# Kernel tuning notes

Measured on AMD Instinct MI355X. Metric: run time of the kernel, lower is better.

The kernel has to match this reference:

```python
import jax, jax.numpy as jnp
import numpy as np

# Model config (matches init_kwargs)
L, B, S, D, H, HKV, HD, FF, V = 2, 1, 2048, 2048, 16, 4, 128, 5632, 32000
EPS = 1e-5
ROPE_BASE = 10000.0


def setup_inputs() -> dict:
    key = jax.random.key(0)
    ks = jax.random.split(key, 13)
    s = 0.02  # init scale keeps activations/softmax numerically sane
    return {
        "idx": jax.random.randint(ks[0], (B, S), 0, V, dtype=jnp.int32),
        "embed": jax.random.normal(ks[1], (V, D), jnp.float32) * s,
        "wq": jax.random.normal(ks[2], (L, D, D), jnp.float32) * s,
        "wk": jax.random.normal(ks[3], (L, D, HKV * HD), jnp.float32) * s,
        "wv": jax.random.normal(ks[4], (L, D, HKV * HD), jnp.float32) * s,
        "wo": jax.random.normal(ks[5], (L, D, D), jnp.float32) * s,
        "ln1_g": jnp.ones((L, D), jnp.float32),
        "ln2_g": jnp.ones((L, D), jnp.float32),
        "w_gate": jax.random.normal(ks[6], (L, D, FF), jnp.float32) * s,
        "w_up": jax.random.normal(ks[7], (L, D, FF), jnp.float32) * s,
        "w_down": jax.random.normal(ks[8], (L, FF, D), jnp.float32) * s,
        "final_g": jnp.ones((D,), jnp.float32),
        "lm_head": jax.random.normal(ks[9], (V, D), jnp.float32) * s,
    }


def _rope_cos_sin(seq_len, n_elem, base=ROPE_BASE):
    inv = 1.0 / base ** (jnp.arange(0, n_elem, 2, dtype=jnp.float32)[: n_elem // 2] / n_elem)
    f = jnp.outer(jnp.arange(seq_len, dtype=jnp.float32), inv)  # [S, HD/2]
    return jnp.cos(f), jnp.sin(f)


def _apply_rope(x, cos, sin):
    # x: [B, S, h, HD]; split last dim into halves (matches torch reshape(...,2,-1))
    d2 = x.shape[-1] // 2
    x1, x2 = x[..., :d2], x[..., d2:]
    c = cos[None, :, None, :]
    s = sin[None, :, None, :]
    return jnp.concatenate([x1 * c - x2 * s, x2 * c + x1 * s], axis=-1)


def _rmsnorm(x, g, eps=EPS):
    return x * jax.lax.rsqrt(jnp.mean(x * x, axis=-1, keepdims=True) + eps) * g


def _forward(idx, embed, wq, wk, wv, wo, ln1_g, ln2_g, w_gate, w_up, w_down, final_g, lm_head):
    cos, sin = _rope_cos_sin(S, HD)
    # NOTE: the original uses a MULTIPLICATIVE bool mask on scores (scores * mask),
    # zeroing (not -inf'ing) future positions before softmax. Replicated faithfully.
    mask = jnp.tril(jnp.ones((S, S), jnp.float32))
    rep = H // HKV
    scale = 1.0 / np.sqrt(HD).astype(np.float32)

    x = embed[idx]  # [B, S, D]

    def layer(x, p):
        lwq, lwk, lwv, lwo, g1, g2, lwg, lwu, lwd = p
        h = _rmsnorm(x, g1)
        q = (h @ lwq).reshape(B, S, H, HD)
        k = (h @ lwk).reshape(B, S, HKV, HD)
        v = (h @ lwv).reshape(B, S, HKV, HD)
        q = _apply_rope(q, cos, sin)
        k = _apply_rope(k, cos, sin)
        k = jnp.repeat(k, rep, axis=2)  # GQA repeat_interleave over heads
        v = jnp.repeat(v, rep, axis=2)
        scores = jnp.einsum("bqhd,bkhd->bhqk", q, k) * scale * mask
        attn = jax.nn.softmax(scores, axis=-1)
        y = jnp.einsum("bhqk,bkhd->bqhd", attn, v).reshape(B, S, D) @ lwo
        x = x + y
        h2 = _rmsnorm(x, g2)
        x = x + (jax.nn.silu(h2 @ lwu) * (h2 @ lwg)) @ lwd
        return x, None

    x, _ = jax.lax.scan(layer, x, (wq, wk, wv, wo, ln1_g, ln2_g, w_gate, w_up, w_down))
    return _rmsnorm(x, final_g) @ lm_head.T  # [B, S, V]


def reference(idx, embed, wq, wk, wv, wo, ln1_g, ln2_g, w_gate, w_up, w_down, final_g, lm_head):
    return _forward(idx, embed, wq, wk, wv, wo, ln1_g, ln2_g, w_gate, w_up, w_down, final_g, lm_head)
```

## Files before the change

### kernel.cpp

```cpp
#include <hip/hip_runtime.h>

#define SQ     2048
#define DMODEL 2048
#define NHEAD  16
#define NKV    4
#define HDIM   128
#define FFDIM  5632
#define VOCAB  32000
#define NLAYER 2
#define EPSV   1e-5f

typedef __bf16 bf16;
typedef __bf16 bf16x4 __attribute__((ext_vector_type(4)));
typedef __bf16 bf16x8 __attribute__((ext_vector_type(8)));
typedef float  f32x4  __attribute__((ext_vector_type(4)));

enum { EP_STOREF = 0, EP_ADD = 2, EP_STOREB = 3, EP_QKV = 6, EP_GLU = 7, EP_ATOMIC = 8 };

#define GLD(gp, lp) __builtin_amdgcn_global_load_lds( \
    (const __attribute__((address_space(1))) void*)(gp), \
    (__attribute__((address_space(3))) void*)(lp), 16, 0, 0)

#define MFMA16(a, b, c) __builtin_amdgcn_mfma_f32_16x16x32_bf16(a, b, c, 0, 0, 0)

#define FENCE() __builtin_amdgcn_sched_barrier(0)
#define PH_BAR() do { FENCE(); __builtin_amdgcn_s_barrier(); FENCE(); } while (0)

#define XCD_SWZ(TM)                                                        \
  const int GM  = (int)gridDim.x;                                          \
  const int nwg = GM * (int)gridDim.y;                                     \
  const int bid = (int)blockIdx.y * GM + (int)blockIdx.x;                  \
  const int q8  = nwg >> 3, r8 = nwg & 7;                                  \
  const int xcd = bid & 7, rnk = bid >> 3;                                 \
  const int swz = ((xcd < r8) ? xcd * (q8 + 1)                             \
                              : r8 * (q8 + 1) + (xcd - r8) * q8) + rnk;    \
  const int m0  = (swz % GM) * (TM);                                       \
  const int n0  = (swz / GM) * (TM == 256 ? 256 : 128);

template<int EPI, int NBUF>
__global__ __launch_bounds__(256, NBUF == 2 ? 2 : 1)
void gemm128(const bf16* __restrict__ A, const bf16* __restrict__ B,
             void* __restrict__ C, const void* __restrict__ Cin,
             bf16* __restrict__ C2, bf16* __restrict__ C3,
             const float* __restrict__ cosT, const float* __restrict__ sinT,
             int K, int lda, int ldb, int ldc)
{
  __shared__ bf16 As[NBUF][128 * 64];
  __shared__ bf16 Bs[NBUF][128 * 64];

  const int tid  = (int)threadIdx.x;
  const int lane = tid & 63;
  const int wave = tid >> 6;
  const int wm   = wave >> 1, wn = wave & 1;

  XCD_SWZ(128)

  const int z    = (int)blockIdx.z;
  const int nkt  = (K >> 6) / (int)gridDim.z;
  const int kt0  = z * nkt;
  const int srow = lane >> 3;
  const long sxcol = (long)(((lane & 7) ^ (lane >> 3)) * 8);
  const int colc = lane & 15;
  const int g4   = lane >> 4;

  auto stage = [&](int t, int buf) {
    if (t < nkt) {
      const long kc = (long)(kt0 + t) * 64 + sxcol;
      bf16* dA = As[buf];
      bf16* dB = Bs[buf];
      #pragma unroll
      for (int c = 0; c < 4; ++c) {
        const int chunk = wave * 4 + c;
        const int row   = chunk * 8 + srow;
        GLD(A + (long)(m0 + row) * lda + kc, dA + chunk * 512);
        GLD(B + (long)(n0 + row) * ldb + kc, dB + chunk * 512);
      }
    }
  };

  stage(0, 0);
  if (NBUF == 3) stage(1, 1);

  f32x4 acc[4][4] = {};
  int wb = (NBUF == 3) ? 2 : 1;
  int rb = 0;

  for (int t = 0; t < nkt; ++t) {
    if (NBUF == 2) {
      stage(t + 1, wb);
      wb ^= 1;
      FENCE();
      if (t + 1 < nkt) asm volatile("s_waitcnt vmcnt(8)" ::: "memory");
      else             asm volatile("s_waitcnt vmcnt(0)" ::: "memory");
    } else {
      stage(t + 2, wb);
      wb = (wb == 2) ? 0 : wb + 1;
      FENCE();
      if (t + 2 < nkt)      asm volatile("s_waitcnt vmcnt(16)" ::: "memory");
      else if (t + 1 < nkt) asm volatile("s_waitcnt vmcnt(8)"  ::: "memory");
      else                  asm volatile("s_waitcnt vmcnt(0)"  ::: "memory");
    }
    PH_BAR();
    const char* Ab = (const char*)As[rb];
    const char* Bb = (const char*)Bs[rb];
    rb = (NBUF == 2) ? (rb ^ 1) : ((rb == 2) ? 0 : rb + 1);
    #pragma unroll
    for (int kk = 0; kk < 2; ++kk) {
      bf16x8 af[4], bv[4];
      #pragma unroll
      for (int m = 0; m < 4; ++m) {
        const int r = wm * 64 + m * 16 + colc;
        af[m] = *(const bf16x8*)(Ab + r * 128 + (((kk * 4 + g4) ^ (r & 7)) * 16));
      }
      #pragma unroll
      for (int n = 0; n < 4; ++n) {
        const int r = n * 32 + wn * 16 + colc;
        bv[n] = *(const bf16x8*)(Bb + r * 128 + (((kk * 4 + g4) ^ (r & 7)) * 16));
      }
      #pragma unroll
      for (int m = 0; m < 4; ++m)
        #pragma unroll
        for (int n = 0; n < 4; ++n)
          acc[m][n] = MFMA16(af[m], bv[n], acc[m][n]);
    }
    PH_BAR();
  }

  if (EPI == EP_QKV && n0 < 2560) {
    #pragma unroll
    for (int m = 0; m < 4; ++m) {
      const int gr0 = m0 + wm * 64 + m * 16 + g4 * 4;
      #pragma unroll
      for (int n = 0; n < 2; ++n) {
        const int i   = n * 32 + wn * 16 + colc;
        const int gc1 = n0 + i;
        #pragma unroll
        for (int r = 0; r < 4; ++r) {
          const int row = gr0 + r;
          const float c  = cosT[row * 64 + i];
          const float sn = sinT[row * 64 + i];
          const float x1 = acc[m][n][r];
          const float x2 = acc[m][n + 2][r];
          const float y1 = x1 * c - x2 * sn;
          const float y2 = x2 * c + x1 * sn;
          if (n0 < 2048) {
            bf16* q = (bf16*)C + (long)row * DMODEL;
            q[gc1] = (bf16)y1; q[gc1 + 64] = (bf16)y2;
          } else {
            bf16* k = C2 + (long)row * 512 + (gc1 - 2048);
            k[0] = (bf16)y1; k[64] = (bf16)y2;
          }
        }
      }
    }
    return;
  }

  #pragma unroll
  for (int m = 0; m < 4; ++m) {
    const int gr0 = m0 + wm * 64 + m * 16 + g4 * 4;
    #pragma unroll
    for (int n = 0; n < 4; ++n) {
      const int gc = n0 + n * 32 + wn * 16 + colc;
      if (EPI == EP_QKV) {
        bf16x4 pk = { (bf16)acc[m][n][0], (bf16)acc[m][n][1],
                      (bf16)acc[m][n][2], (bf16)acc[m][n][3] };
        *(bf16x4*)(C3 + (long)(gc - 2560) * SQ + gr0) = pk;
      } else if (EPI == EP_GLU) {
        #pragma unroll
        for (int r = 0; r < 4; ++r) {
          const float v = acc[m][n][r];
          const float o = __shfl_xor(v, 1);
          if ((colc & 1) == 0) {
            const float res = (o / (1.0f + __expf(-o))) * v;
            ((bf16*)C)[(long)(gr0 + r) * ldc + (gc >> 1)] = (bf16)res;
          }
        }
      } else if (EPI == EP_ATOMIC) {
        #pragma unroll
        for (int r = 0; r < 4; ++r)
          unsafeAtomicAdd((float*)C + (long)(gr0 + r) * ldc + gc, acc[m][n][r]);
      } else {
        #pragma unroll
        for (int r = 0; r < 4; ++r) {
          const long off = (long)(gr0 + r) * ldc + gc;
          const float v = acc[m][n][r];
          if (EPI == EP_STOREF)      ((float*)C)[off] = v;
          else if (EPI == EP_ADD)    ((float*)C)[off] = ((const float*)Cin)[off] + v;
          else if (EPI == EP_STOREB) ((bf16*)C)[off] = (bf16)v;
        }
      }
    }
  }
}

template<int EPI>
__global__ __launch_bounds__(512, 2)
void gemm256(const bf16* __restrict__ A, const bf16* __restrict__ B,
             void* __restrict__ C, const void* __restrict__ Cin,
             int K, int lda, int ldb, int ldc)
{
  __shared__ bf16 smem[2][4][128 * 64];

  const int tid  = (int)threadIdx.x;
  const int lane = tid & 63;
  const int wave = tid >> 6;
  const int wm   = wave >> 2;
  const int wn   = wave & 3;

  XCD_SWZ(256)

  const int nkt  = K >> 6;
  const int srow = lane >> 3;
  const long sxcol = (long)(((lane & 7) ^ (lane >> 3)) * 8);
  const int frow = lane & 15;
  const int ph0  = ((     (lane >> 4)) ^ (lane & 7)) * 16;
  const int ph1  = ((4 + (lane >> 4)) ^ (lane & 7)) * 16;

  auto stageA = [&](int tile, int half) {
    if (tile < nkt) {
      const long kc = (long)tile * 64 + sxcol;
      #pragma unroll
      for (int i = 0; i < 2; ++i)
        GLD(A + (long)(m0 + half * 128 + wave * 16 + i * 8 + srow) * lda + kc,
            smem[tile & 1][half] + (wave * 16 + i * 8) * 64);
    }
  };
  auto stageB = [&](int tile, int half) {
    if (tile < nkt) {
      const long kc = (long)tile * 64 + sxcol;
      #pragma unroll
      for (int i = 0; i < 2; ++i)
        GLD(B + (long)(n0 + half * 128 + wave * 16 + i * 8 + srow) * ldb + kc,
            smem[tile & 1][2 + half] + (wave * 16 + i * 8) * 64);
    }
  };

  stageB(0, 0); stageB(0, 1); stageA(0, 0); stageA(0, 1);
  asm volatile("s_waitcnt vmcnt(4)" ::: "memory");
  stageB(1, 0); stageB(1, 1); stageA(1, 0);
  asm volatile("s_waitcnt vmcnt(6)" ::: "memory");
  PH_BAR();

  f32x4 acc[8][4] = {};

  for (int t = 0; t < nkt; ++t) {
    const int bsel = t & 1;
    const char* Asl = (const char*)smem[bsel][wm];
    const char* Bsl = (const char*)smem[bsel][2 + (wn >> 1)];
    const int brow = (wn & 1) * 64;

    bf16x8 ar[4][2], b0f[2][2], b1f[2][2];

    #pragma unroll
    for (int mr = 0; mr < 4; ++mr) {
      ar[mr][0] = *(const bf16x8*)(Asl + (mr * 16 + frow) * 128 + ph0);
      ar[mr][1] = *(const bf16x8*)(Asl + (mr * 16 + frow) * 128 + ph1);
    }
    #pragma unroll
    for (int nc = 0; nc < 2; ++nc) {
      b0f[nc][0] = *(const bf16x8*)(Bsl + (brow + nc * 16 + frow) * 128 + ph0);
      b0f[nc][1] = *(const bf16x8*)(Bsl + (brow + nc * 16 + frow) * 128 + ph1);
    }
    stageA(t + 1, 1);
    PH_BAR();
    __builtin_amdgcn_s_setprio(1);
    #pragma unroll
    for (int mr = 0; mr < 4; ++mr)
      #pragma unroll
      for (int nc = 0; nc < 2; ++nc) {
        acc[mr][nc] = MFMA16(ar[mr][0], b0f[nc][0], acc[mr][nc]);
        acc[mr][nc] = MFMA16(ar[mr][1], b0f[nc][1], acc[mr][nc]);
      }
    __builtin_amdgcn_s_setprio(0);
    PH_BAR();

    #pragma unroll
    for (int nc = 0; nc < 2; ++nc) {
      b1f[nc][0] = *(const bf16x8*)(Bsl + (brow + (2 + nc) * 16 + frow) * 128 + ph0);
      b1f[nc][1] = *(const bf16x8*)(Bsl + (brow + (2 + nc) * 16 + frow) * 128 + ph1);
    }
    PH_BAR();
    __builtin_amdgcn_s_setprio(1);
    #pragma unroll
    for (int mr = 0; mr < 4; ++mr)
      #pragma unroll
      for (int nc = 0; nc < 2; ++nc) {
        acc[mr][2 + nc] = MFMA16(ar[mr][0], b1f[nc][0], acc[mr][2 + nc]);
        acc[mr][2 + nc] = MFMA16(ar[mr][1], b1f[nc][1], acc[mr][2 + nc]);
      }
    __builtin_amdgcn_s_setprio(0);
    PH_BAR();

    #pragma unroll
    for (int mr = 0; mr < 4; ++mr) {
      ar[mr][0] = *(const bf16x8*)(Asl + ((4 + mr) * 16 + frow) * 128 + ph0);
      ar[mr][1] = *(const bf16x8*)(Asl + ((4 + mr) * 16 + frow) * 128 + ph1);
    }
    stageB(t + 2, 0); stageB(t + 2, 1);
    PH_BAR();
    __builtin_amdgcn_s_setprio(1);
    #pragma unroll
    for (int mr = 0; mr < 4; ++mr)
      #pragma unroll
      for (int nc = 0; nc < 2; ++nc) {
        acc[4 + mr][nc] = MFMA16(ar[mr][0], b0f[nc][0], acc[4 + mr][nc]);
        acc[4 + mr][nc] = MFMA16(ar[mr][1], b0f[nc][1], acc[4 + mr][nc]);
      }
    __builtin_amdgcn_s_setprio(0);
    PH_BAR();

    stageA(t + 2, 0);
    PH_BAR();
    __builtin_amdgcn_s_setprio(1);
    #pragma unroll
    for (int mr = 0; mr < 4; ++mr)
      #pragma unroll
      for (int nc = 0; nc < 2; ++nc) {
        acc[4 + mr][2 + nc] = MFMA16(ar[mr][0], b1f[nc][0], acc[4 + mr][2 + nc]);
        acc[4 + mr][2 + nc] = MFMA16(ar[mr][1], b1f[nc][1], acc[4 + mr][2 + nc]);
      }
    __builtin_amdgcn_s_setprio(0);
    FENCE();
    if (t + 2 < nkt) asm volatile("s_waitcnt vmcnt(6)" ::: "memory");
    else             asm volatile("s_waitcnt vmcnt(0)" ::: "memory");
    PH_BAR();
  }

  #pragma unroll
  for (int mr = 0; mr < 8; ++mr) {
    const int gr0 = m0 + wm * 128 + mr * 16 + (lane >> 4) * 4;
    #pragma unroll
    for (int nc = 0; nc < 4; ++nc) {
      const int gc = n0 + wn * 64 + nc * 16 + (lane & 15);
      #pragma unroll
      for (int r = 0; r < 4; ++r) {
        const long off = (long)(gr0 + r) * ldc + gc;
        const float v = acc[mr][nc][r];
        if (EPI == EP_STOREF)      ((float*)C)[off] = v;
        else if (EPI == EP_STOREB) ((bf16*)C)[off] = (bf16)v;
      }
    }
  }
}

__global__ __launch_bounds__(256, 1)
void flash_attn(const bf16* __restrict__ qb, const bf16* __restrict__ kb,
                const bf16* __restrict__ vT, const float* __restrict__ suffPc,
                bf16* __restrict__ yb, float scale)
{
  __shared__ bf16 Ks[128 * 128];
  __shared__ bf16 Vs[128 * 128];
  __shared__ bf16 Ps[128 * 136];

  const int tid  = (int)threadIdx.x;
  const int lane = tid & 63;
  const int w    = tid >> 6;
  const int qt   = (int)blockIdx.x;
  const int h    = (int)blockIdx.y;
  const int kvh  = h >> 2;

  const int l15 = lane & 15;
  const int g4  = lane >> 4;

  bf16x8 qf[2][4];
  #pragma unroll
  for (int m = 0; m < 2; ++m)
    #pragma unroll
    for (int ks = 0; ks < 4; ++ks)
      qf[m][ks] = *(const bf16x8*)(qb + (long)(qt * 128 + w * 32 + m * 16 + l15) * DMODEL
                                   + h * HDIM + ks * 32 + g4 * 8);

  f32x4 acc_o[2][8] = {};
  float den[2][4] = {};

  const bf16* Kg = kb + (long)kvh * HDIM;
  const bf16* Vg = vT + (long)(kvh * HDIM) * SQ;

  for (int j = 0; j <= qt; ++j) {
    const bool diag = (j == qt);
    PH_BAR();

    #pragma unroll
    for (int i = 0; i < 8; ++i) {
      const int rb = w * 32 + i * 4;
      const int r  = rb + g4;
      GLD(Kg + (long)(j * 128 + r) * 512 + ((l15 ^ (r & 7)) * 8), Ks + rb * 128);
    }
    #pragma unroll
    for (int i = 0; i < 8; ++i) {
      const int rb = w * 32 + i * 4;
      const int r  = rb + g4;
      GLD(Vg + (long)r * SQ + j * 128 + ((l15 ^ (r & 7)) * 8), Vs + rb * 128);
    }
    asm volatile("s_waitcnt vmcnt(8)" ::: "memory");
    PH_BAR();

    f32x4 acc_s[2][8] = {};
    #pragma unroll
    for (int ks = 0; ks < 4; ++ks) {
      bf16x8 kf[8];
      #pragma unroll
      for (int n = 0; n < 8; ++n) {
        const int kr = n * 16 + l15;
        kf[n] = *(const bf16x8*)((const char*)Ks + kr * 256 + (((ks * 4 + g4) ^ (kr & 7)) * 16));
      }
      #pragma unroll
      for (int m = 0; m < 2; ++m)
        #pragma unroll
        for (int n = 0; n < 8; ++n)
          acc_s[m][n] = MFMA16(qf[m][ks], kf[n], acc_s[m][n]);
    }

    float rs[2][4] = {};
    #pragma unroll
    for (int m = 0; m < 2; ++m)
      #pragma unroll
      for (int n = 0; n < 8; ++n) {
        const int kc = n * 16 + l15;
        #pragma unroll
        for (int r = 0; r < 4; ++r) {
          const int qlr = w * 32 + m * 16 + g4 * 4 + r;
          float p = __expf(acc_s[m][n][r] * scale);
          if (diag && kc > qlr) p = 1.0f;
          rs[m][r] += p;
          Ps[(w * 32 + m * 16 + g4 * 4 + r) * 136 + kc] = (bf16)p;
        }
      }
    #pragma unroll
    for (int m = 0; m < 2; ++m)
      #pragma unroll
      for (int r = 0; r < 4; ++r) {
        float v = rs[m][r];
        v += __shfl_xor(v, 1); v += __shfl_xor(v, 2);
        v += __shfl_xor(v, 4); v += __shfl_xor(v, 8);
        den[m][r] += v;
      }

    asm volatile("s_waitcnt vmcnt(0) lgkmcnt(0)" ::: "memory");
    PH_BAR();

    #pragma unroll
    for (int ks = 0; ks < 4; ++ks) {
      bf16x8 pa[2], vf[8];
      #pragma unroll
      for (int m = 0; m < 2; ++m)
        pa[m] = *(const bf16x8*)((const char*)Ps + (w * 32 + m * 16 + l15) * 272
                                 + ks * 64 + g4 * 16);
      #pragma unroll
      for (int n = 0; n < 8; ++n) {
        const int dr = n * 16 + l15;
        vf[n] = *(const bf16x8*)((const char*)Vs + dr * 256 + (((ks * 4 + g4) ^ (dr & 7)) * 16));
      }
      #pragma unroll
      for (int m = 0; m < 2; ++m)
        #pragma unroll
        for (int n = 0; n < 8; ++n)
          acc_o[m][n] = MFMA16(pa[m], vf[n], acc_o[m][n]);
    }
  }

  float denf[2][4];
  #pragma unroll
  for (int m = 0; m < 2; ++m)
    #pragma unroll
    for (int r = 0; r < 4; ++r)
      denf[m][r] = den[m][r] + 128.0f * (15 - qt);

  #pragma unroll
  for (int n = 0; n < 8; ++n) {
    const float t = suffPc[((kvh << 4) + qt) * 128 + n * 16 + l15];
    #pragma unroll
    for (int m = 0; m < 2; ++m)
      #pragma unroll
      for (int r = 0; r < 4; ++r) {
        const float y = (acc_o[m][n][r] + t) / denf[m][r];
        yb[(long)(qt * 128 + w * 32 + m * 16 + g4 * 4 + r) * DMODEL
           + h * HDIM + n * 16 + l15] = (bf16)y;
      }
  }
}

__global__ __launch_bounds__(128)
void vchunksum(const bf16* __restrict__ vT, float* __restrict__ chunkS)
{
  const int kvh = (int)blockIdx.x;
  const int c   = (int)blockIdx.y;
  const int d   = (int)threadIdx.x;
  const bf16* row = vT + (long)(kvh * HDIM + d) * SQ + c * 128;
  float s = 0.f;
  #pragma unroll
  for (int r = 0; r < 16; ++r) {
    bf16x8 v = *(const bf16x8*)(row + r * 8);
    #pragma unroll
    for (int e = 0; e < 8; ++e) s += (float)v[e];
  }
  chunkS[(kvh * 16 + c) * 128 + d] = s;
}

__global__ __launch_bounds__(128)
void vsuffscan(const float* __restrict__ chunkS, float* __restrict__ suffPc)
{
  const int kvh = (int)blockIdx.x;
  const int d   = (int)threadIdx.x;
  float a = 0.f;
  for (int c = 15; c >= 0; --c) {
    suffPc[(kvh * 16 + c) * 128 + d] = a;
    a += chunkS[(kvh * 16 + c) * 128 + d];
  }
}

__global__ __launch_bounds__(256)
void transpose_cvt3(const float* __restrict__ s0, bf16* __restrict__ d0, int N0, int L0,
                    const float* __restrict__ s1, bf16* __restrict__ d1, int N1, int L1,
                    const float* __restrict__ s2, bf16* __restrict__ d2, int N2, int L2,
                    int K)
{
  const float* src; bf16* dst; int N, L;
  if (blockIdx.z == 0)      { src = s0; dst = d0; N = N0; L = L0; }
  else if (blockIdx.z == 1) { src = s1; dst = d1; N = N1; L = L1; }
  else                      { src = s2; dst = d2; N = N2; L = L2; }
  if (!src) return;
  const int n0 = (int)blockIdx.x * 32; if (n0 >= N) return;
  const int k0 = (int)blockIdx.y * 32;
  __shared__ float t[32][33];
  const int tr = (int)threadIdx.x >> 3;
  const int tc = ((int)threadIdx.x & 7) * 4;
  f32x4 v = *(const f32x4*)(src + (long)(k0 + tr) * N + n0 + tc);
  t[tr][tc] = v[0]; t[tr][tc + 1] = v[1]; t[tr][tc + 2] = v[2]; t[tr][tc + 3] = v[3];
  __syncthreads();
  bf16x4 b = { (bf16)t[tc][tr], (bf16)t[tc + 1][tr], (bf16)t[tc + 2][tr], (bf16)t[tc + 3][tr] };
  *(bf16x4*)(dst + (long)(n0 + tr) * L + k0 + tc) = b;
}

__global__ __launch_bounds__(256)
void cvt_bf16_kernel(const float* __restrict__ in, bf16* __restrict__ out, int nvec)
{
  const int i = (int)(blockIdx.x * 256 + threadIdx.x);
  if (i < nvec) {
    f32x4 v = ((const f32x4*)in)[i];
    bf16x4 b = { (bf16)v[0], (bf16)v[1], (bf16)v[2], (bf16)v[3] };
    ((bf16x4*)out)[i] = b;
  }
}

__global__ __launch_bounds__(256)
void rmsnorm_kernel(bf16* __restrict__ out, const float* __restrict__ in, const float* __restrict__ g)
{
  const int row = (int)blockIdx.x;
  const float* x = in + (long)row * DMODEL;
  bf16* o = out + (long)row * DMODEL;
  const int tid = (int)threadIdx.x;
  f32x4 v0 = *(const f32x4*)(x + tid * 4);
  f32x4 v1 = *(const f32x4*)(x + tid * 4 + 1024);
  float ss = v0[0]*v0[0] + v0[1]*v0[1] + v0[2]*v0[2] + v0[3]*v0[3]
           + v1[0]*v1[0] + v1[1]*v1[1] + v1[2]*v1[2] + v1[3]*v1[3];
  #pragma unroll
  for (int o_ = 32; o_; o_ >>= 1) ss += __shfl_xor(ss, o_);
  __shared__ float sm[4];
  if ((tid & 63) == 0) sm[tid >> 6] = ss;
  __syncthreads();
  ss = sm[0] + sm[1] + sm[2] + sm[3];
  const float r = 1.0f / sqrtf(ss * (1.0f / DMODEL) + EPSV);
  f32x4 g0 = *(const f32x4*)(g + tid * 4);
  f32x4 g1 = *(const f32x4*)(g + tid * 4 + 1024);
  bf16x4 o0, o1;
  #pragma unroll
  for (int j = 0; j < 4; ++j) { o0[j] = (bf16)(v0[j] * r * g0[j]); o1[j] = (bf16)(v1[j] * r * g1[j]); }
  *(bf16x4*)(o + tid * 4) = o0;
  *(bf16x4*)(o + tid * 4 + 1024) = o1;
}

__global__ void rope_tables(float* cosT, float* sinT)
{
  const int s = (int)blockIdx.x;
  const int i = (int)threadIdx.x;
  const double inv = pow(10000.0, -(double)i / 64.0);
  const double f = (double)s * inv;
  cosT[s * 64 + i] = (float)cos(f);
  sinT[s * 64 + i] = (float)sin(f);
}

__global__ __launch_bounds__(256)
void embed_gather(f32x4* x, const f32x4* embed, const int* idx)
{
  const int t = (int)(blockIdx.x * 256 + threadIdx.x);
  const int s = t >> 9;
  const int c = t & 511;
  x[t] = embed[(long)idx[s] * 512 + c];
}

extern "C" void kernel_launch(void* const* d_in, const int* in_sizes, int n_in,
                              void* d_out, int out_size, void* d_ws, size_t ws_size,
                              hipStream_t stream)
{
  (void)in_sizes; (void)n_in; (void)out_size;
  const int*   idx   = (const int*)  d_in[0];
  const float* embed = (const float*)d_in[1];
  const float* wq    = (const float*)d_in[2];
  const float* wk    = (const float*)d_in[3];
  const float* wv    = (const float*)d_in[4];
  const float* wo    = (const float*)d_in[5];
  const float* ln1g  = (const float*)d_in[6];
  const float* ln2g  = (const float*)d_in[7];
  const float* wgate = (const float*)d_in[8];
  const float* wup   = (const float*)d_in[9];
  const float* wdown = (const float*)d_in[10];
  const float* fing  = (const float*)d_in[11];
  const float* lmh   = (const float*)d_in[12];
  float* out = (float*)d_out;

  char* wp = (char*)d_ws;
  auto alloc = [&](size_t bytes) { char* p = wp; wp += (bytes + 255) & ~(size_t)255; return p; };
  float* cosT   = (float*)alloc((size_t)SQ * 64 * 4);
  float* sinT   = (float*)alloc((size_t)SQ * 64 * 4);
  float* suffPc = (float*)alloc((size_t)NKV * 16 * 128 * 4);
  float* chunkS = (float*)alloc((size_t)NKV * 16 * 128 * 4);
  float* x      = (float*)alloc((size_t)SQ * DMODEL * 4);
  bf16*  h      = (bf16*) alloc((size_t)SQ * DMODEL * 2);
  bf16*  qb     = (bf16*) alloc((size_t)SQ * DMODEL * 2);
  bf16*  kb     = (bf16*) alloc((size_t)SQ * 512 * 2);
  bf16*  vT     = (bf16*) alloc((size_t)512 * SQ * 2);
  bf16*  ffb    = (bf16*) alloc((size_t)SQ * FFDIM * 2);
  size_t used  = (size_t)(wp - (char*)d_ws);
  bf16*  wbuf  = (bf16*)wp;
  size_t avail = ws_size - used;

  bf16* yb = qb;
  const float scale = 0.08838834764831845f;

  rope_tables<<<SQ, 64, 0, stream>>>(cosT, sinT);
  embed_gather<<<(SQ * 512) / 256, 256, 0, stream>>>((f32x4*)x, (const f32x4*)embed, idx);

  for (int l = 0; l < NLAYER; ++l) {
    const float* lwq = wq    + (long)l * DMODEL * DMODEL;
    const float* lwk = wk    + (long)l * DMODEL * 512;
    const float* lwv = wv    + (long)l * DMODEL * 512;
    const float* lwo = wo    + (long)l * DMODEL * DMODEL;
    const float* lwg = wgate + (long)l * DMODEL * FFDIM;
    const float* lwu = wup   + (long)l * DMODEL * FFDIM;
    const float* lwd = wdown + (long)l * FFDIM * DMODEL;

    rmsnorm_kernel<<<SQ, 256, 0, stream>>>(h, x, ln1g + l * DMODEL);

    transpose_cvt3<<<dim3(64, 64, 3), 256, 0, stream>>>(
        lwq, wbuf, DMODEL, DMODEL,
        lwk, wbuf + (long)2048 * DMODEL, 512, DMODEL,
        lwv, wbuf + (long)2560 * DMODEL, 512, DMODEL, DMODEL);
    gemm128<EP_QKV, 2><<<dim3(16, 24), 256, 0, stream>>>(
        h, wbuf, qb, nullptr, kb, vT, cosT, sinT, DMODEL, DMODEL, DMODEL, 0);

    vchunksum<<<dim3(NKV, 16), 128, 0, stream>>>(vT, chunkS);
    vsuffscan<<<NKV, 128, 0, stream>>>(chunkS, suffPc);

    flash_attn<<<dim3(16, NHEAD), 256, 0, stream>>>(qb, kb, vT, suffPc, yb, scale);

    transpose_cvt3<<<dim3(64, 64, 1), 256, 0, stream>>>(
        lwo, wbuf, DMODEL, DMODEL,
        nullptr, nullptr, 0, 0, nullptr, nullptr, 0, 0, DMODEL);
    gemm128<EP_ATOMIC, 2><<<dim3(16, 16, 2), 256, 0, stream>>>(
        yb, wbuf, x, nullptr, nullptr, nullptr, nullptr, nullptr,
        DMODEL, DMODEL, DMODEL, DMODEL);

    rmsnorm_kernel<<<SQ, 256, 0, stream>>>(h, x, ln2g + l * DMODEL);

    transpose_cvt3<<<dim3(176, 64, 2), 256, 0, stream>>>(
        lwg, wbuf, FFDIM, 2 * DMODEL,
        lwu, wbuf + DMODEL, FFDIM, 2 * DMODEL,
        nullptr, nullptr, 0, 0, DMODEL);
    gemm128<EP_GLU, 2><<<dim3(16, 88), 256, 0, stream>>>(
        h, wbuf, ffb, nullptr, nullptr, nullptr, nullptr, nullptr,
        DMODEL, DMODEL, DMODEL, FFDIM);

    transpose_cvt3<<<dim3(64, 176, 1), 256, 0, stream>>>(
        lwd, wbuf, DMODEL, FFDIM,
        nullptr, nullptr, 0, 0, nullptr, nullptr, 0, 0, FFDIM);
    gemm128<EP_ATOMIC, 2><<<dim3(16, 16, 2), 256, 0, stream>>>(
        ffb, wbuf, x, nullptr, nullptr, nullptr, nullptr, nullptr,
        FFDIM, FFDIM, FFDIM, DMODEL);
  }

  rmsnorm_kernel<<<SQ, 256, 0, stream>>>(h, x, fing);

  long chunkRows = (long)(avail / ((size_t)DMODEL * 2)) & ~255L;
  if (chunkRows > VOCAB) chunkRows = VOCAB;
  for (long c0 = 0; c0 < VOCAB; c0 += chunkRows) {
    const long rows = (VOCAB - c0 < chunkRows) ? (VOCAB - c0) : chunkRows;
    const int  nvec = (int)(rows * DMODEL / 4);
    cvt_bf16_kernel<<<(nvec + 255) / 256, 256, 0, stream>>>(lmh + c0 * DMODEL, wbuf, nvec);
    gemm256<EP_STOREF><<<dim3(8, (int)(rows / 256)), 512, 0, stream>>>(
        h, wbuf, out + c0, nullptr, DMODEL, DMODEL, DMODEL, VOCAB);
  }
}
```

Baseline: 1.212 ms.

## Reuse K LDS buffer for P in flash attention and batch Wo conversion

Flash attention no longer has a separate P scratch buffer. P is written into the K tile's shared memory after a barrier, which frees LDS, and launch bounds are raised so two blocks can share a CU. Separately, the Wo weight transpose/convert is folded into the Q/K/V conversion launch and written to its own region of the buffer, removing one kernel launch per layer. The cost is an extra barrier per KV tile and tighter register limits, which could cause spills.

```diff
diff --git a/kernel.cpp b/kernel.cpp
--- a/kernel.cpp
+++ b/kernel.cpp
@@ -344,14 +344,13 @@
   }
 }
 
-__global__ __launch_bounds__(256, 1)
+__global__ __launch_bounds__(256, 2)
 void flash_attn(const bf16* __restrict__ qb, const bf16* __restrict__ kb,
                 const bf16* __restrict__ vT, const float* __restrict__ suffPc,
                 bf16* __restrict__ yb, float scale)
 {
   __shared__ bf16 Ks[128 * 128];
   __shared__ bf16 Vs[128 * 128];
-  __shared__ bf16 Ps[128 * 136];
 
   const int tid  = (int)threadIdx.x;
   const int lane = tid & 63;
@@ -412,6 +411,9 @@
           acc_s[m][n] = MFMA16(qf[m][ks], kf[n], acc_s[m][n]);
     }
 
+    asm volatile("s_waitcnt lgkmcnt(0)" ::: "memory");
+    PH_BAR();
+
     float rs[2][4] = {};
     #pragma unroll
     for (int m = 0; m < 2; ++m)
@@ -420,11 +422,12 @@
         const int kc = n * 16 + l15;
         #pragma unroll
         for (int r = 0; r < 4; ++r) {
-          const int qlr = w * 32 + m * 16 + g4 * 4 + r;
+          const int prow = w * 32 + m * 16 + g4 * 4 + r;
           float p = __expf(acc_s[m][n][r] * scale);
-          if (diag && kc > qlr) p = 1.0f;
+          if (diag && kc > prow) p = 1.0f;
           rs[m][r] += p;
-          Ps[(w * 32 + m * 16 + g4 * 4 + r) * 136 + kc] = (bf16)p;
+          *(bf16*)((char*)Ks + prow * 256
+                   + (((kc >> 3) ^ (prow & 7)) * 16) + (kc & 7) * 2) = (bf16)p;
         }
       }
     #pragma unroll
@@ -444,9 +447,10 @@
     for (int ks = 0; ks < 4; ++ks) {
       bf16x8 pa[2], vf[8];
       #pragma unroll
-      for (int m = 0; m < 2; ++m)
-        pa[m] = *(const bf16x8*)((const char*)Ps + (w * 32 + m * 16 + l15) * 272
-                                 + ks * 64 + g4 * 16);
+      for (int m = 0; m < 2; ++m) {
+        const int pr = w * 32 + m * 16 + l15;
+        pa[m] = *(const bf16x8*)((const char*)Ks + pr * 256 + (((ks * 4 + g4) ^ (pr & 7)) * 16));
+      }
       #pragma unroll
       for (int n = 0; n < 8; ++n) {
         const int dr = n * 16 + l15;
@@ -511,15 +515,17 @@
 }
 
 __global__ __launch_bounds__(256)
-void transpose_cvt3(const float* __restrict__ s0, bf16* __restrict__ d0, int N0, int L0,
+void transpose_cvt4(const float* __restrict__ s0, bf16* __restrict__ d0, int N0, int L0,
                     const float* __restrict__ s1, bf16* __restrict__ d1, int N1, int L1,
                     const float* __restrict__ s2, bf16* __restrict__ d2, int N2, int L2,
+                    const float* __restrict__ s3, bf16* __restrict__ d3, int N3, int L3,
                     int K)
 {
   const float* src; bf16* dst; int N, L;
   if (blockIdx.z == 0)      { src = s0; dst = d0; N = N0; L = L0; }
   else if (blockIdx.z == 1) { src = s1; dst = d1; N = N1; L = L1; }
-  else                      { src = s2; dst = d2; N = N2; L = L2; }
+  else if (blockIdx.z == 2) { src = s2; dst = d2; N = N2; L = L2; }
+  else                      { src = s3; dst = d3; N = N3; L = L3; }
   if (!src) return;
   const int n0 = (int)blockIdx.x * 32; if (n0 >= N) return;
   const int k0 = (int)blockIdx.y * 32;
@@ -643,10 +649,12 @@
 
     rmsnorm_kernel<<<SQ, 256, 0, stream>>>(h, x, ln1g + l * DMODEL);
 
-    transpose_cvt3<<<dim3(64, 64, 3), 256, 0, stream>>>(
+    bf16* wob = wbuf + (long)3072 * DMODEL;
+    transpose_cvt4<<<dim3(64, 64, 4), 256, 0, stream>>>(
         lwq, wbuf, DMODEL, DMODEL,
         lwk, wbuf + (long)2048 * DMODEL, 512, DMODEL,
-        lwv, wbuf + (long)2560 * DMODEL, 512, DMODEL, DMODEL);
+        lwv, wbuf + (long)2560 * DMODEL, 512, DMODEL,
+        lwo, wob, DMODEL, DMODEL, DMODEL);
     gemm128<EP_QKV, 2><<<dim3(16, 24), 256, 0, stream>>>(
         h, wbuf, qb, nullptr, kb, vT, cosT, sinT, DMODEL, DMODEL, DMODEL, 0);
 
@@ -655,26 +663,24 @@
 
     flash_attn<<<dim3(16, NHEAD), 256, 0, stream>>>(qb, kb, vT, suffPc, yb, scale);
 
-    transpose_cvt3<<<dim3(64, 64, 1), 256, 0, stream>>>(
-        lwo, wbuf, DMODEL, DMODEL,
-        nullptr, nullptr, 0, 0, nullptr, nullptr, 0, 0, DMODEL);
     gemm128<EP_ATOMIC, 2><<<dim3(16, 16, 2), 256, 0, stream>>>(
-        yb, wbuf, x, nullptr, nullptr, nullptr, nullptr, nullptr,
+        yb, wob, x, nullptr, nullptr, nullptr, nullptr, nullptr,
         DMODEL, DMODEL, DMODEL, DMODEL);
 
     rmsnorm_kernel<<<SQ, 256, 0, stream>>>(h, x, ln2g + l * DMODEL);
 
-    transpose_cvt3<<<dim3(176, 64, 2), 256, 0, stream>>>(
+    transpose_cvt4<<<dim3(176, 64, 2), 256, 0, stream>>>(
         lwg, wbuf, FFDIM, 2 * DMODEL,
         lwu, wbuf + DMODEL, FFDIM, 2 * DMODEL,
-        nullptr, nullptr, 0, 0, DMODEL);
+        nullptr, nullptr, 0, 0, nullptr, nullptr, 0, 0, DMODEL);
     gemm128<EP_GLU, 2><<<dim3(16, 88), 256, 0, stream>>>(
         h, wbuf, ffb, nullptr, nullptr, nullptr, nullptr, nullptr,
         DMODEL, DMODEL, DMODEL, FFDIM);
 
-    transpose_cvt3<<<dim3(64, 176, 1), 256, 0, stream>>>(
+    transpose_cvt4<<<dim3(64, 176, 1), 256, 0, stream>>>(
         lwd, wbuf, DMODEL, FFDIM,
-        nullptr, nullptr, 0, 0, nullptr, nullptr, 0, 0, FFDIM);
+        nullptr, nullptr, 0, 0, nullptr, nullptr, 0, 0,
+        nullptr, nullptr, 0, 0, FFDIM);
     gemm128<EP_ATOMIC, 2><<<dim3(16, 16, 2), 256, 0, stream>>>(
         ffb, wbuf, x, nullptr, nullptr, nullptr, nullptr, nullptr,
         FFDIM, FFDIM, FFDIM, DMODEL);
```

Result: slower. 1.376 ms (+13.5%).
